# Performance work log

Measured on AMD Instinct MI355X. Metric: run time of the kernel, lower is better.

Reference implementation:

```python
import jax, jax.numpy as jnp
import numpy as np
import math

THETA = 10000.0

def apply_rope(x):
    # x: [B, H, S, D] with D even; interleaved even/odd rotation
    B, H, S, D = x.shape
    dim_half = D // 2
    freq_idx = jnp.arange(dim_half, dtype=jnp.float32)
    inv_freq = jnp.exp(-math.log(THETA) * freq_idx * 2.0 / D)  # [D/2]
    pos = jnp.arange(S, dtype=jnp.float32)
    angles = pos[:, None] * inv_freq[None, :]      # [S, D/2]
    cos = jnp.cos(angles)[None, None]              # [1,1,S,D/2]
    sin = jnp.sin(angles)[None, None]
    x_even = x[..., ::2]
    x_odd = x[..., 1::2]
    r_even = x_even * cos - x_odd * sin
    r_odd = x_odd * cos + x_even * sin
    return jnp.stack([r_even, r_odd], axis=-1).reshape(B, H, S, D)

def setup_inputs() -> dict:
    key = jax.random.key(0)
    ks = jax.random.split(key, 5)
    B, S, E = 2, 2048, 1024
    std = 0.02
    inp = {
        "hidden_states": jax.random.normal(ks[0], (B, S, E), dtype=jnp.float32),
        "Wq": jax.random.normal(ks[1], (E, E), dtype=jnp.float32) * std,
        "bq": jnp.zeros((E,), dtype=jnp.float32),
        "Wk": jax.random.normal(ks[2], (E, E), dtype=jnp.float32) * std,
        "bk": jnp.zeros((E,), dtype=jnp.float32),
        "Wv": jax.random.normal(ks[3], (E, E), dtype=jnp.float32) * std,
        "bv": jnp.zeros((E,), dtype=jnp.float32),
        "Wo": jax.random.normal(ks[4], (E, E), dtype=jnp.float32) * std,
        "bo": jnp.zeros((E,), dtype=jnp.float32),
    }
    return inp

def reference(hidden_states, Wq, bq, Wk, bk, Wv, bv, Wo, bo):
    NUM_HEADS = 16
    B, S, E = hidden_states.shape
    D = E // NUM_HEADS
    scale = 1.0 / math.sqrt(D)

    def proj(W, b):
        # torch Linear: x @ W.T + b; then [B,S,H,D] -> [B,H,S,D]
        y = hidden_states @ W.T + b
        return y.reshape(B, S, NUM_HEADS, D).transpose(0, 2, 1, 3)

    q = apply_rope(proj(Wq, bq))
    k = apply_rope(proj(Wk, bk))
    v = proj(Wv, bv)

    scores = jnp.einsum("bhqd,bhkd->bhqk", q, k) * scale
    attn = jax.nn.softmax(scores, axis=-1)
    out = jnp.einsum("bhqk,bhkd->bhqd", attn, v)  # [B,H,S,D]
    out = out.transpose(0, 2, 1, 3).reshape(B, S, E)
    return out @ Wo.T + bo  # dropout: eval mode (identity)
```

## Files before the change

kernel.cpp:

```cpp
#include <hip/hip_runtime.h>
#include <math.h>

#define B_ 2
#define S_ 2048
#define E_ 1024
#define H_ 16
#define D_ 64
#define M_ (B_*S_)

typedef short bf16x8 __attribute__((ext_vector_type(8)));
typedef float f32x4 __attribute__((ext_vector_type(4)));
typedef unsigned short u16x4 __attribute__((ext_vector_type(4)));

__device__ __forceinline__ unsigned short f2bf(float f) {
    unsigned int u = __builtin_bit_cast(unsigned int, f);
    u += 0x7FFFu + ((u >> 16) & 1u);
    return (unsigned short)(u >> 16);
}
__device__ __forceinline__ f32x4 mfma16(bf16x8 a, bf16x8 b, f32x4 c) {
    return __builtin_amdgcn_mfma_f32_16x16x32_bf16(a, b, c, 0, 0, 0);
}
__device__ __forceinline__ bf16x8 cvt8(const float* p) {
    f32x4 lo = *(const f32x4*)p;
    f32x4 hi = *(const f32x4*)(p + 4);
    bf16x8 r;
#pragma unroll
    for (int e = 0; e < 4; e++) { r[e] = (short)f2bf(lo[e]); r[e + 4] = (short)f2bf(hi[e]); }
    return r;
}

__global__ __launch_bounds__(256, 3) void qkv_rope_kernel(
    const float* __restrict__ X,
    const float* __restrict__ Wq, const float* __restrict__ Wk,
    const float* __restrict__ Wv,
    const float* __restrict__ bq, const float* __restrict__ bk,
    const float* __restrict__ bv,
    unsigned short* __restrict__ Qo, unsigned short* __restrict__ Ko,
    unsigned short* __restrict__ Vo)
{
    __shared__ __align__(16) unsigned char lds_raw[128 * 132 * 2];
    unsigned short* As = (unsigned short*)lds_raw;
    unsigned short* Bs = (unsigned short*)(lds_raw + 8192);
    unsigned short* Cs = (unsigned short*)lds_raw;

    const int t = threadIdx.x;
    const int w = t >> 6, lane = t & 63, quad = lane >> 4, l16 = lane & 15;
    const int wr = (w >> 1) * 64, wc = (w & 1) * 64;
    const int n0 = blockIdx.x * 128, m0 = blockIdx.y * 128;
    const int z = blockIdx.z;
    const float* W    = (z == 0) ? Wq : (z == 1) ? Wk : Wv;
    const float* bias = (z == 0) ? bq : (z == 1) ? bk : bv;

    const int r4 = t >> 2, c8 = (t & 3) * 8;
    const float* Ag = X + (size_t)(m0 + r4) * E_ + c8;
    const float* Bg = W + (size_t)(n0 + r4) * E_ + c8;

    f32x4 zero = {0.f, 0.f, 0.f, 0.f};
    f32x4 acc[4][4];
#pragma unroll
    for (int i = 0; i < 4; i++)
#pragma unroll
        for (int j = 0; j < 4; j++) acc[i][j] = zero;

    for (int kt = 0; kt < E_; kt += 32) {
        bf16x8 a0 = cvt8(Ag + kt);
        bf16x8 a1 = cvt8(Ag + 64 * E_ + kt);
        bf16x8 b0 = cvt8(Bg + kt);
        bf16x8 b1 = cvt8(Bg + 64 * E_ + kt);
        __syncthreads();
        *(bf16x8*)&As[t * 8]        = a0;
        *(bf16x8*)&As[t * 8 + 2048] = a1;
        *(bf16x8*)&Bs[t * 8]        = b0;
        *(bf16x8*)&Bs[t * 8 + 2048] = b1;
        __syncthreads();
        bf16x8 af[4], bfr[4];
#pragma unroll
        for (int i = 0; i < 4; i++)
            af[i] = *(const bf16x8*)&As[(wr + i * 16 + l16) * 32 + quad * 8];
#pragma unroll
        for (int j = 0; j < 4; j++)
            bfr[j] = *(const bf16x8*)&Bs[(wc + j * 16 + l16) * 32 + quad * 8];
#pragma unroll
        for (int i = 0; i < 4; i++)
#pragma unroll
            for (int j = 0; j < 4; j++)
                acc[i][j] = mfma16(af[i], bfr[j], acc[i][j]);
    }

    __syncthreads();
    const int seg = quad;
    if (z < 2) {
        const float C = -0.41524101186091903f;
        const float INV2PI = 0.15915494309189535f;
#pragma unroll
        for (int j = 0; j < 4; j++) {
            int n_local = wc + j * 16 + l16;
            int n = n0 + n_local;
            int d = n & 63, f = d >> 1;
            float inv_rev = exp2f(C * (float)f) * INV2PI;
            float bvv = bias[n];
            float sgn = (d & 1) ? 1.f : -1.f;
#pragma unroll
            for (int i = 0; i < 4; i++) {
                int mb = wr + i * 16 + quad * 4;
#pragma unroll
                for (int r = 0; r < 4; r++) {
                    int m = m0 + mb + r;
                    int s = m & (S_ - 1);
                    float val = acc[i][j][r] + bvv;
                    float oth = __shfl_xor(val, 1);
                    float rev = (float)s * inv_rev;
                    float fr = rev - rintf(rev);
                    float sn = __builtin_amdgcn_sinf(fr);
                    float cs = __builtin_amdgcn_cosf(fr);
                    Cs[(mb + r) * 132 + n_local] = f2bf(val * cs + sgn * oth * sn);
                }
            }
        }
        __syncthreads();
        unsigned short* Out = (z == 0) ? Qo : Ko;
        const int btok = m0 >> 11;
        const int half = seg & 1;
#pragma unroll
        for (int it = 0; it < 16; it++) {
            int m_local = it * 8 + w * 2 + (seg >> 1);
            int s = (m0 + m_local) & (S_ - 1);
            int h = (n0 + half * 64) >> 6;
            u16x4 v = *(const u16x4*)&Cs[m_local * 132 + half * 64 + l16 * 4];
            *(u16x4*)&Out[(((size_t)btok * H_ + h) * S_ + s) * D_ + l16 * 4] = v;
        }
    } else {
#pragma unroll
        for (int j = 0; j < 4; j++) {
            int n_local = wc + j * 16 + l16;
            float bvv = bias[n0 + n_local];
#pragma unroll
            for (int i = 0; i < 4; i++) {
                int mb = wr + i * 16 + quad * 4;
#pragma unroll
                for (int r = 0; r < 4; r++)
                    Cs[n_local * 132 + mb + r] = f2bf(acc[i][j][r] + bvv);
            }
        }
        __syncthreads();
        const int btok = m0 >> 11;
        const int s0 = m0 & (S_ - 1);
        const int half = seg & 1;
#pragma unroll
        for (int it = 0; it < 16; it++) {
            int n_local = it * 8 + w * 2 + (seg >> 1);
            int n = n0 + n_local;
            int h = n >> 6, d = n & 63;
            u16x4 v = *(const u16x4*)&Cs[n_local * 132 + half * 64 + l16 * 4];
            *(u16x4*)&Vo[(((size_t)btok * H_ + h) * D_ + d) * S_ + s0 + half * 64 + l16 * 4] = v;
        }
    }
}

__global__ __launch_bounds__(256, 2) void attn_kernel(
    const unsigned short* __restrict__ Q, const unsigned short* __restrict__ K,
    const unsigned short* __restrict__ Vt, unsigned short* __restrict__ ctx)
{
    __shared__ unsigned short Ks[2][64 * 32];
    __shared__ unsigned short Vs[2][64 * 32];
    __shared__ unsigned short Ps[4][32 * 72];
    const int t = threadIdx.x;
    const int w = t >> 6, lane = t & 63, quad = lane >> 4, l16 = lane & 15;
    const int bh = blockIdx.y;
    const int q0 = blockIdx.x * 128 + w * 32;

    const unsigned short* Qg = Q + ((size_t)bh * S_ + q0) * D_;
    bf16x8 qf[2][2];
#pragma unroll
    for (int i = 0; i < 2; i++)
#pragma unroll
        for (int ks = 0; ks < 2; ks++)
            qf[i][ks] = *(const bf16x8*)(Qg + (i * 16 + l16) * 64 + ks * 32 + quad * 8);

    bf16x8 ones;
#pragma unroll
    for (int e = 0; e < 8; e++) ones[e] = (short)0x3F80;

    f32x4 zero = {0.f, 0.f, 0.f, 0.f};
    f32x4 acc_o[2][4];
    f32x4 acc_l[2];
#pragma unroll
    for (int i = 0; i < 2; i++) {
        acc_l[i] = zero;
#pragma unroll
        for (int j = 0; j < 4; j++) acc_o[i][j] = zero;
    }

    const int r4 = t >> 2, c8v = (t & 3) * 8;
    const unsigned short* Kg0 = K + (size_t)bh * S_ * D_;
    const unsigned short* Vg0 = Vt + (size_t)bh * D_ * S_;

    for (int kt = 0; kt < S_; kt += 64) {
        const unsigned short* Kg = Kg0 + (size_t)(kt + r4) * 64 + c8v;
        const unsigned short* Vg = Vg0 + (size_t)r4 * S_ + kt + c8v;
        bf16x8 k0 = *(const bf16x8*)(Kg);
        bf16x8 k1 = *(const bf16x8*)(Kg + 32);
        bf16x8 v0 = *(const bf16x8*)(Vg);
        bf16x8 v1 = *(const bf16x8*)(Vg + 32);
        __syncthreads();
        *(bf16x8*)&Ks[0][t * 8] = k0;
        *(bf16x8*)&Ks[1][t * 8] = k1;
        *(bf16x8*)&Vs[0][t * 8] = v0;
        *(bf16x8*)&Vs[1][t * 8] = v1;
        __syncthreads();

        f32x4 sc[2][4];
#pragma unroll
        for (int i = 0; i < 2; i++)
#pragma unroll
            for (int j = 0; j < 4; j++) sc[i][j] = zero;
#pragma unroll
        for (int ks = 0; ks < 2; ks++) {
            bf16x8 kf[4];
#pragma unroll
            for (int j = 0; j < 4; j++)
                kf[j] = *(const bf16x8*)&Ks[ks][(j * 16 + l16) * 32 + quad * 8];
#pragma unroll
            for (int i = 0; i < 2; i++)
#pragma unroll
                for (int j = 0; j < 4; j++)
                    sc[i][j] = mfma16(qf[i][ks], kf[j], sc[i][j]);
        }
#pragma unroll
        for (int i = 0; i < 2; i++)
#pragma unroll
            for (int j = 0; j < 4; j++)
#pragma unroll
                for (int r = 0; r < 4; r++) {
                    float p = __expf(sc[i][j][r] * 0.125f);
                    Ps[w][(i * 16 + quad * 4 + r) * 72 + j * 16 + l16] = f2bf(p);
                }
        __syncthreads();
#pragma unroll
        for (int ks = 0; ks < 2; ks++) {
            bf16x8 pf[2], vf[4];
#pragma unroll
            for (int i = 0; i < 2; i++)
                pf[i] = *(const bf16x8*)&Ps[w][(i * 16 + l16) * 72 + ks * 32 + quad * 8];
#pragma unroll
            for (int jd = 0; jd < 4; jd++)
                vf[jd] = *(const bf16x8*)&Vs[ks][(jd * 16 + l16) * 32 + quad * 8];
#pragma unroll
            for (int i = 0; i < 2; i++) {
#pragma unroll
                for (int jd = 0; jd < 4; jd++)
                    acc_o[i][jd] = mfma16(pf[i], vf[jd], acc_o[i][jd]);
                acc_l[i] = mfma16(pf[i], ones, acc_l[i]);
            }
        }
    }

    const int b = bh >> 4, h = bh & 15;
#pragma unroll
    for (int i = 0; i < 2; i++) {
        f32x4 rl;
#pragma unroll
        for (int r = 0; r < 4; r++) rl[r] = 1.0f / acc_l[i][r];
#pragma unroll
        for (int jd = 0; jd < 4; jd++)
#pragma unroll
            for (int r = 0; r < 4; r++) {
                int qrow = q0 + i * 16 + quad * 4 + r;
                int col = h * 64 + jd * 16 + l16;
                ctx[((size_t)b * S_ + qrow) * E_ + col] = f2bf(acc_o[i][jd][r] * rl[r]);
            }
    }
}

__global__ __launch_bounds__(256, 2) void out_kernel(
    const unsigned short* __restrict__ Cx, const float* __restrict__ Wo,
    const float* __restrict__ bo, float* __restrict__ out)
{
    __shared__ unsigned short As[128 * 32];
    __shared__ unsigned short Bs[64 * 32];
    const int t = threadIdx.x;
    const int w = t >> 6, lane = t & 63, quad = lane >> 4, l16 = lane & 15;
    const int m0 = blockIdx.y * 128, n0 = blockIdx.x * 64;
    const int wr = w * 32;
    const int r4 = t >> 2, c8 = (t & 3) * 8;
    const unsigned short* Ag = Cx + (size_t)(m0 + r4) * E_ + c8;
    const float*          Bg = Wo + (size_t)(n0 + (r4 & 63)) * E_ + c8;

    f32x4 zero = {0.f, 0.f, 0.f, 0.f};
    f32x4 acc[2][4];
#pragma unroll
    for (int i = 0; i < 2; i++)
#pragma unroll
        for (int j = 0; j < 4; j++) acc[i][j] = zero;

    for (int kt = 0; kt < E_; kt += 32) {
        bf16x8 a0 = *(const bf16x8*)(Ag + kt);
        bf16x8 a1 = *(const bf16x8*)(Ag + 64 * E_ + kt);
        bf16x8 b0 = cvt8(Bg + kt);
        __syncthreads();
        *(bf16x8*)&As[t * 8]        = a0;
        *(bf16x8*)&As[t * 8 + 2048] = a1;
        *(bf16x8*)&Bs[t * 8]        = b0;
        __syncthreads();
        bf16x8 af[2], bfr[4];
#pragma unroll
        for (int i = 0; i < 2; i++)
            af[i] = *(const bf16x8*)&As[(wr + i * 16 + l16) * 32 + quad * 8];
#pragma unroll
        for (int j = 0; j < 4; j++)
            bfr[j] = *(const bf16x8*)&Bs[(j * 16 + l16) * 32 + quad * 8];
#pragma unroll
        for (int i = 0; i < 2; i++)
#pragma unroll
            for (int j = 0; j < 4; j++)
                acc[i][j] = mfma16(af[i], bfr[j], acc[i][j]);
    }

#pragma unroll
    for (int j = 0; j < 4; j++) {
        int n = n0 + j * 16 + l16;
        float bvv = bo[n];
#pragma unroll
        for (int i = 0; i < 2; i++) {
            int mrow = m0 + wr + i * 16 + quad * 4;
#pragma unroll
            for (int r = 0; r < 4; r++)
                out[(size_t)(mrow + r) * E_ + n] = acc[i][j][r] + bvv;
        }
    }
}

extern "C" void kernel_launch(void* const* d_in, const int* in_sizes, int n_in,
                              void* d_out, int out_size, void* d_ws, size_t ws_size,
                              hipStream_t stream) {
    const float* X  = (const float*)d_in[0];
    const float* Wq = (const float*)d_in[1];
    const float* bq = (const float*)d_in[2];
    const float* Wk = (const float*)d_in[3];
    const float* bk = (const float*)d_in[4];
    const float* Wv = (const float*)d_in[5];
    const float* bv = (const float*)d_in[6];
    const float* Wo = (const float*)d_in[7];
    const float* bo = (const float*)d_in[8];
    float* outp = (float*)d_out;

    const size_t TN = (size_t)B_ * H_ * S_ * D_;
    if (ws_size < 4 * TN * sizeof(unsigned short)) return;

    unsigned short* Qb = (unsigned short*)d_ws;
    unsigned short* Kb = Qb + TN;
    unsigned short* Vb = Kb + TN;
    unsigned short* Cx = Vb + TN;

    qkv_rope_kernel<<<dim3(E_ / 128, M_ / 128, 3), 256, 0, stream>>>(
        X, Wq, Wk, Wv, bq, bk, bv, Qb, Kb, Vb);
    attn_kernel<<<dim3(S_ / 128, B_ * H_), 256, 0, stream>>>(Qb, Kb, Vb, Cx);
    out_kernel<<<dim3(E_ / 64, M_ / 128), 256, 0, stream>>>(Cx, Wo, bo, outp);
}
```

Baseline: 220.5 us.

## Pad LDS tiles against bank conflicts and retile attention to 16 rows per wave

All three kernels now pad their shared-memory GEMM tiles to a row stride of 36 bf16 instead of 32. This is meant to cut LDS bank conflicts on the strided MFMA fragment reads. The attention kernel now gives each wave 16 query rows instead of 32, doubling the grid and raising the launch-bounds occupancy hint from 2 to 4. It also drops the block barrier between the per-wave P write and read, since that buffer is private to each wave. In exchange, K/V tiles are reused across fewer query rows, so global and LDS traffic per unit of compute rises in attention.

```diff
diff --git a/kernel.cpp b/kernel.cpp
--- a/kernel.cpp
+++ b/kernel.cpp
@@ -40,7 +40,7 @@
 {
     __shared__ __align__(16) unsigned char lds_raw[128 * 132 * 2];
     unsigned short* As = (unsigned short*)lds_raw;
-    unsigned short* Bs = (unsigned short*)(lds_raw + 8192);
+    unsigned short* Bs = (unsigned short*)(lds_raw + 9216);
     unsigned short* Cs = (unsigned short*)lds_raw;
 
     const int t = threadIdx.x;
@@ -52,6 +52,7 @@
     const float* bias = (z == 0) ? bq : (z == 1) ? bk : bv;
 
     const int r4 = t >> 2, c8 = (t & 3) * 8;
+    const int st = r4 * 36 + c8;
     const float* Ag = X + (size_t)(m0 + r4) * E_ + c8;
     const float* Bg = W + (size_t)(n0 + r4) * E_ + c8;
 
@@ -68,18 +69,18 @@
         bf16x8 b0 = cvt8(Bg + kt);
         bf16x8 b1 = cvt8(Bg + 64 * E_ + kt);
         __syncthreads();
-        *(bf16x8*)&As[t * 8]        = a0;
-        *(bf16x8*)&As[t * 8 + 2048] = a1;
-        *(bf16x8*)&Bs[t * 8]        = b0;
-        *(bf16x8*)&Bs[t * 8 + 2048] = b1;
+        *(bf16x8*)&As[st]           = a0;
+        *(bf16x8*)&As[st + 64 * 36] = a1;
+        *(bf16x8*)&Bs[st]           = b0;
+        *(bf16x8*)&Bs[st + 64 * 36] = b1;
         __syncthreads();
         bf16x8 af[4], bfr[4];
 #pragma unroll
         for (int i = 0; i < 4; i++)
-            af[i] = *(const bf16x8*)&As[(wr + i * 16 + l16) * 32 + quad * 8];
+            af[i] = *(const bf16x8*)&As[(wr + i * 16 + l16) * 36 + quad * 8];
 #pragma unroll
         for (int j = 0; j < 4; j++)
-            bfr[j] = *(const bf16x8*)&Bs[(wc + j * 16 + l16) * 32 + quad * 8];
+            bfr[j] = *(const bf16x8*)&Bs[(wc + j * 16 + l16) * 36 + quad * 8];
 #pragma unroll
         for (int i = 0; i < 4; i++)
 #pragma unroll
@@ -157,41 +158,36 @@
     }
 }
 
-__global__ __launch_bounds__(256, 2) void attn_kernel(
+__global__ __launch_bounds__(256, 4) void attn_kernel(
     const unsigned short* __restrict__ Q, const unsigned short* __restrict__ K,
     const unsigned short* __restrict__ Vt, unsigned short* __restrict__ ctx)
 {
-    __shared__ unsigned short Ks[2][64 * 32];
-    __shared__ unsigned short Vs[2][64 * 32];
-    __shared__ unsigned short Ps[4][32 * 72];
+    __shared__ unsigned short Ks[2][64 * 36];
+    __shared__ unsigned short Vs[2][64 * 36];
+    __shared__ unsigned short Ps[4][16 * 72];
     const int t = threadIdx.x;
     const int w = t >> 6, lane = t & 63, quad = lane >> 4, l16 = lane & 15;
     const int bh = blockIdx.y;
-    const int q0 = blockIdx.x * 128 + w * 32;
+    const int q0 = blockIdx.x * 64 + w * 16;
 
     const unsigned short* Qg = Q + ((size_t)bh * S_ + q0) * D_;
-    bf16x8 qf[2][2];
-#pragma unroll
-    for (int i = 0; i < 2; i++)
-#pragma unroll
-        for (int ks = 0; ks < 2; ks++)
-            qf[i][ks] = *(const bf16x8*)(Qg + (i * 16 + l16) * 64 + ks * 32 + quad * 8);
+    bf16x8 qf[2];
+#pragma unroll
+    for (int ks = 0; ks < 2; ks++)
+        qf[ks] = *(const bf16x8*)(Qg + (size_t)l16 * 64 + ks * 32 + quad * 8);
 
     bf16x8 ones;
 #pragma unroll
     for (int e = 0; e < 8; e++) ones[e] = (short)0x3F80;
 
     f32x4 zero = {0.f, 0.f, 0.f, 0.f};
-    f32x4 acc_o[2][4];
-    f32x4 acc_l[2];
-#pragma unroll
-    for (int i = 0; i < 2; i++) {
-        acc_l[i] = zero;
-#pragma unroll
-        for (int j = 0; j < 4; j++) acc_o[i][j] = zero;
-    }
+    f32x4 acc_o[4];
+    f32x4 acc_l = zero;
+#pragma unroll
+    for (int j = 0; j < 4; j++) acc_o[j] = zero;
 
     const int r4 = t >> 2, c8v = (t & 3) * 8;
+    const int st = r4 * 36 + c8v;
     const unsigned short* Kg0 = K + (size_t)bh * S_ * D_;
     const unsigned short* Vg0 = Vt + (size_t)bh * D_ * S_;
 
@@ -203,86 +199,68 @@
         bf16x8 v0 = *(const bf16x8*)(Vg);
         bf16x8 v1 = *(const bf16x8*)(Vg + 32);
         __syncthreads();
-        *(bf16x8*)&Ks[0][t * 8] = k0;
-        *(bf16x8*)&Ks[1][t * 8] = k1;
-        *(bf16x8*)&Vs[0][t * 8] = v0;
-        *(bf16x8*)&Vs[1][t * 8] = v1;
-        __syncthreads();
-
-        f32x4 sc[2][4];
-#pragma unroll
-        for (int i = 0; i < 2; i++)
-#pragma unroll
-            for (int j = 0; j < 4; j++) sc[i][j] = zero;
+        *(bf16x8*)&Ks[0][st] = k0;
+        *(bf16x8*)&Ks[1][st] = k1;
+        *(bf16x8*)&Vs[0][st] = v0;
+        *(bf16x8*)&Vs[1][st] = v1;
+        __syncthreads();
+
+        f32x4 sc[4];
+#pragma unroll
+        for (int j = 0; j < 4; j++) sc[j] = zero;
 #pragma unroll
         for (int ks = 0; ks < 2; ks++) {
-            bf16x8 kf[4];
-#pragma unroll
-            for (int j = 0; j < 4; j++)
-                kf[j] = *(const bf16x8*)&Ks[ks][(j * 16 + l16) * 32 + quad * 8];
-#pragma unroll
-            for (int i = 0; i < 2; i++)
-#pragma unroll
-                for (int j = 0; j < 4; j++)
-                    sc[i][j] = mfma16(qf[i][ks], kf[j], sc[i][j]);
-        }
-#pragma unroll
-        for (int i = 0; i < 2; i++)
-#pragma unroll
-            for (int j = 0; j < 4; j++)
-#pragma unroll
-                for (int r = 0; r < 4; r++) {
-                    float p = __expf(sc[i][j][r] * 0.125f);
-                    Ps[w][(i * 16 + quad * 4 + r) * 72 + j * 16 + l16] = f2bf(p);
-                }
-        __syncthreads();
+#pragma unroll
+            for (int j = 0; j < 4; j++) {
+                bf16x8 kf = *(const bf16x8*)&Ks[ks][(j * 16 + l16) * 36 + quad * 8];
+                sc[j] = mfma16(qf[ks], kf, sc[j]);
+            }
+        }
+#pragma unroll
+        for (int j = 0; j < 4; j++)
+#pragma unroll
+            for (int r = 0; r < 4; r++) {
+                float p = __expf(sc[j][r] * 0.125f);
+                Ps[w][(quad * 4 + r) * 72 + j * 16 + l16] = f2bf(p);
+            }
 #pragma unroll
         for (int ks = 0; ks < 2; ks++) {
-            bf16x8 pf[2], vf[4];
-#pragma unroll
-            for (int i = 0; i < 2; i++)
-                pf[i] = *(const bf16x8*)&Ps[w][(i * 16 + l16) * 72 + ks * 32 + quad * 8];
-#pragma unroll
-            for (int jd = 0; jd < 4; jd++)
-                vf[jd] = *(const bf16x8*)&Vs[ks][(jd * 16 + l16) * 32 + quad * 8];
-#pragma unroll
-            for (int i = 0; i < 2; i++) {
-#pragma unroll
-                for (int jd = 0; jd < 4; jd++)
-                    acc_o[i][jd] = mfma16(pf[i], vf[jd], acc_o[i][jd]);
-                acc_l[i] = mfma16(pf[i], ones, acc_l[i]);
-            }
+            bf16x8 pf = *(const bf16x8*)&Ps[w][l16 * 72 + ks * 32 + quad * 8];
+#pragma unroll
+            for (int jd = 0; jd < 4; jd++) {
+                bf16x8 vf = *(const bf16x8*)&Vs[ks][(jd * 16 + l16) * 36 + quad * 8];
+                acc_o[jd] = mfma16(pf, vf, acc_o[jd]);
+            }
+            acc_l = mfma16(pf, ones, acc_l);
         }
     }
 
     const int b = bh >> 4, h = bh & 15;
-#pragma unroll
-    for (int i = 0; i < 2; i++) {
-        f32x4 rl;
-#pragma unroll
-        for (int r = 0; r < 4; r++) rl[r] = 1.0f / acc_l[i][r];
-#pragma unroll
-        for (int jd = 0; jd < 4; jd++)
-#pragma unroll
-            for (int r = 0; r < 4; r++) {
-                int qrow = q0 + i * 16 + quad * 4 + r;
-                int col = h * 64 + jd * 16 + l16;
-                ctx[((size_t)b * S_ + qrow) * E_ + col] = f2bf(acc_o[i][jd][r] * rl[r]);
-            }
-    }
+    f32x4 rl;
+#pragma unroll
+    for (int r = 0; r < 4; r++) rl[r] = 1.0f / acc_l[r];
+#pragma unroll
+    for (int jd = 0; jd < 4; jd++)
+#pragma unroll
+        for (int r = 0; r < 4; r++) {
+            int qrow = q0 + quad * 4 + r;
+            int col = h * 64 + jd * 16 + l16;
+            ctx[((size_t)b * S_ + qrow) * E_ + col] = f2bf(acc_o[jd][r] * rl[r]);
+        }
 }
 
 __global__ __launch_bounds__(256, 2) void out_kernel(
     const unsigned short* __restrict__ Cx, const float* __restrict__ Wo,
     const float* __restrict__ bo, float* __restrict__ out)
 {
-    __shared__ unsigned short As[128 * 32];
-    __shared__ unsigned short Bs[64 * 32];
+    __shared__ unsigned short As[128 * 36];
+    __shared__ unsigned short Bs[64 * 36];
     const int t = threadIdx.x;
     const int w = t >> 6, lane = t & 63, quad = lane >> 4, l16 = lane & 15;
     const int m0 = blockIdx.y * 128, n0 = blockIdx.x * 64;
     const int wr = w * 32;
     const int r4 = t >> 2, c8 = (t & 3) * 8;
+    const int st = r4 * 36 + c8;
     const unsigned short* Ag = Cx + (size_t)(m0 + r4) * E_ + c8;
     const float*          Bg = Wo + (size_t)(n0 + (r4 & 63)) * E_ + c8;
 
@@ -298,17 +276,17 @@
         bf16x8 a1 = *(const bf16x8*)(Ag + 64 * E_ + kt);
         bf16x8 b0 = cvt8(Bg + kt);
         __syncthreads();
-        *(bf16x8*)&As[t * 8]        = a0;
-        *(bf16x8*)&As[t * 8 + 2048] = a1;
-        *(bf16x8*)&Bs[t * 8]        = b0;
+        *(bf16x8*)&As[st]           = a0;
+        *(bf16x8*)&As[st + 64 * 36] = a1;
+        *(bf16x8*)&Bs[st]           = b0;
         __syncthreads();
         bf16x8 af[2], bfr[4];
 #pragma unroll
         for (int i = 0; i < 2; i++)
-            af[i] = *(const bf16x8*)&As[(wr + i * 16 + l16) * 32 + quad * 8];
+            af[i] = *(const bf16x8*)&As[(wr + i * 16 + l16) * 36 + quad * 8];
 #pragma unroll
         for (int j = 0; j < 4; j++)
-            bfr[j] = *(const bf16x8*)&Bs[(j * 16 + l16) * 32 + quad * 8];
+            bfr[j] = *(const bf16x8*)&Bs[(j * 16 + l16) * 36 + quad * 8];
 #pragma unroll
         for (int i = 0; i < 2; i++)
 #pragma unroll
@@ -354,6 +332,6 @@
 
     qkv_rope_kernel<<<dim3(E_ / 128, M_ / 128, 3), 256, 0, stream>>>(
         X, Wq, Wk, Wv, bq, bk, bv, Qb, Kb, Vb);
-    attn_kernel<<<dim3(S_ / 128, B_ * H_), 256, 0, stream>>>(Qb, Kb, Vb, Cx);
+    attn_kernel<<<dim3(S_ / 64, B_ * H_), 256, 0, stream>>>(Qb, Kb, Vb, Cx);
     out_kernel<<<dim3(E_ / 64, M_ / 128), 256, 0, stream>>>(Cx, Wo, bo, outp);
 }
```

Result: slower. 319.8 us (+45.1%).
